# Kernel optimization log

Hardware: AMD Instinct MI355X
Metric: run time of the kernel (lower is better)

Reference implementation:

```python
import jax, jax.numpy as jnp
import numpy as np
import math

D_MODEL = 1024
MEM_SIZE = 4096
N_HEADS = 8
BATCH = 4
SEQ = 1024
TOP_K = min(SEQ, MEM_SIZE // 10)  # 409, matches torch: min(seq_len, memory_size//10)
UPDATE_RATE = 0.01


def _gelu(x):
    return jax.nn.gelu(x, approximate=False)  # torch nn.GELU default (erf)


def setup_inputs() -> dict:
    key = jax.random.key(0)
    ks = jax.random.split(key, 26)
    w = lambda k, shape, s=0.02: (jax.random.normal(k, shape, jnp.float32) * s)
    inp = {
        "x": jax.random.normal(ks[0], (BATCH, SEQ, D_MODEL), jnp.float32),
        "memory_bank": jax.random.normal(ks[1], (MEM_SIZE, D_MODEL), jnp.float32) * 0.1,
        "memory_indices": jax.random.randint(ks[2], (BATCH, TOP_K), 0, MEM_SIZE, jnp.int32),
        # memory_encoder: Linear -> GELU -> Linear
        "enc_w1": w(ks[3], (D_MODEL, D_MODEL)), "enc_b1": jnp.zeros((D_MODEL,), jnp.float32),
        "enc_w2": w(ks[4], (D_MODEL, D_MODEL)), "enc_b2": jnp.zeros((D_MODEL,), jnp.float32),
        # MultiheadAttention in/out projections
        "wq": w(ks[5], (D_MODEL, D_MODEL)), "bq": jnp.zeros((D_MODEL,), jnp.float32),
        "wk": w(ks[6], (D_MODEL, D_MODEL)), "bk": jnp.zeros((D_MODEL,), jnp.float32),
        "wv": w(ks[7], (D_MODEL, D_MODEL)), "bv": jnp.zeros((D_MODEL,), jnp.float32),
        "wo": w(ks[8], (D_MODEL, D_MODEL)), "bo": jnp.zeros((D_MODEL,), jnp.float32),
        # memory_decoder: Linear -> GELU -> Linear
        "dec_w1": w(ks[9], (D_MODEL, D_MODEL)), "dec_b1": jnp.zeros((D_MODEL,), jnp.float32),
        "dec_w2": w(ks[10], (D_MODEL, D_MODEL)), "dec_b2": jnp.zeros((D_MODEL,), jnp.float32),
        # LayerNorm
        "ln_g": jnp.ones((D_MODEL,), jnp.float32), "ln_b": jnp.zeros((D_MODEL,), jnp.float32),
        # importance_scorer: Linear(d,64) -> GELU -> Linear(64,1) -> Sigmoid
        "imp_w1": w(ks[11], (D_MODEL, 64)), "imp_b1": jnp.zeros((64,), jnp.float32),
        "imp_w2": w(ks[12], (64, 1)), "imp_b2": jnp.zeros((1,), jnp.float32),
    }
    return inp


def reference(x, memory_bank, memory_indices,
              enc_w1, enc_b1, enc_w2, enc_b2,
              wq, bq, wk, bk, wv, bv, wo, bo,
              dec_w1, dec_b1, dec_w2, dec_b2,
              ln_g, ln_b, imp_w1, imp_b1, imp_w2, imp_b2):
    B, L, D = x.shape
    M = memory_bank.shape[0]
    H = N_HEADS
    dh = D // H

    # memory_encoder (dropout inactive at eval)
    enc = _gelu(x @ enc_w1 + enc_b1) @ enc_w2 + enc_b2  # [B,L,D]

    # cross-attention: query = encoded input, key/value = memory bank (shared across batch)
    q = (enc @ wq + bq).reshape(B, L, H, dh)
    k = (memory_bank @ wk + bk).reshape(M, H, dh)
    v = (memory_bank @ wv + bv).reshape(M, H, dh)
    scores = jnp.einsum('blhd,mhd->bhlm', q, k) * (1.0 / math.sqrt(dh))
    attn = jax.nn.softmax(scores, axis=-1)                 # [B,H,L,M]
    ctx = jnp.einsum('bhlm,mhd->blhd', attn, v).reshape(B, L, D)
    mem_out = ctx @ wo + bo

    # memory_decoder + residual + LayerNorm
    dec = _gelu(mem_out @ dec_w1 + dec_b1) @ dec_w2 + dec_b2
    comb = x + dec
    mu = jnp.mean(comb, axis=-1, keepdims=True)
    var = jnp.var(comb, axis=-1, keepdims=True)
    out = (comb - mu) / jnp.sqrt(var + 1e-5) * ln_g + ln_b  # [B,L,D]

    # _update_memory: importance top-k select + sequential EMA scatter into memory bank
    imp = jax.nn.sigmoid(_gelu(x @ imp_w1 + imp_b1) @ imp_w2 + imp_b2)[..., 0]  # [B,L]
    _, top_idx = jax.lax.top_k(imp, TOP_K)                  # [B,K]
    top_tok = jnp.take_along_axis(x, top_idx[..., None], axis=1)  # [B,K,D]

    # faithful to the torch double loop (b outer, k inner): sequential EMA with
    # chained updates on index collisions
    flat_idx = memory_indices.reshape(-1)
    flat_tok = top_tok.reshape(-1, D)

    def body(mem, xs):
        i, t = xs
        row = (1.0 - UPDATE_RATE) * mem[i] + UPDATE_RATE * t
        return mem.at[i].set(row), None

    new_mem, _ = jax.lax.scan(body, memory_bank, (flat_idx, flat_tok))
    return out, new_mem
```

## Files before the change

### kernel.cpp

```cpp
#include <hip/hip_runtime.h>

typedef unsigned short u16;
typedef __attribute__((ext_vector_type(4))) int i4;
typedef __attribute__((ext_vector_type(4))) unsigned u4;
typedef __attribute__((ext_vector_type(4))) unsigned short us4;
typedef __attribute__((ext_vector_type(8))) short short8;
typedef __attribute__((ext_vector_type(4))) float f4;

#define D_MODEL 1024
#define ROWS 4096
#define NHEAD 8
#define DH 128
#define TOPK 409
#define NUPD 1636
#define NBATCH 4
#define MAXC 64
#define NPART 2
#define MRANGE 2048
#define ATTNROWS 32768

__device__ __forceinline__ u16 f2bf(float f) {
  unsigned u = __builtin_bit_cast(unsigned, f);
  u += 0x7fffu + ((u >> 16) & 1u);
  return (u16)(u >> 16);
}
__device__ __forceinline__ float bf2f(u16 b) {
  unsigned u = ((unsigned)b) << 16;
  return __builtin_bit_cast(float, u);
}
__device__ __forceinline__ float gelu_f(float v) {
  return 0.5f * v * (1.0f + erff(v * 0.70710678118654752f));
}
__device__ __forceinline__ void gload16(const void* g, void* l) {
  __builtin_amdgcn_global_load_lds((const __attribute__((address_space(1))) void*)g,
                                   (__attribute__((address_space(3))) void*)l, 16, 0, 0);
}

__global__ __launch_bounds__(256) void conv_kernel(const float* __restrict__ in,
                                                   u16* __restrict__ out, int n4) {
  int i = blockIdx.x * 256 + threadIdx.x;
  if (i < n4) {
    f4 v = ((const f4*)in)[i];
    us4 o;
    o.x = f2bf(v.x); o.y = f2bf(v.y); o.z = f2bf(v.z); o.w = f2bf(v.w);
    ((us4*)out)[i] = o;
  }
}

__global__ __launch_bounds__(256) void wtrans8_kernel(const float* s0, const float* s1,
                                                      const float* s2, const float* s3,
                                                      const float* s4, const float* s5,
                                                      const float* s6, const float* s7,
                                                      u16* __restrict__ dst) {
  const float* srcs[8] = {s0, s1, s2, s3, s4, s5, s6, s7};
  const float* w = srcs[blockIdx.z];
  u16* wt = dst + (size_t)blockIdx.z * (1024 * 1024);
  __shared__ float t[32][33];
  int tx = threadIdx.x & 31, ty = threadIdx.x >> 5;
  int k0 = blockIdx.y * 32, n0 = blockIdx.x * 32;
  for (int r = 0; r < 4; ++r)
    t[ty + r * 8][tx] = w[(size_t)(k0 + ty + r * 8) * 1024 + n0 + tx];
  __syncthreads();
  for (int r = 0; r < 4; ++r)
    wt[(size_t)(n0 + ty + r * 8) * 1024 + k0 + tx] = f2bf(t[tx][ty + r * 8]);
}

template <int EPI>
__global__ __launch_bounds__(256) void gemm_bt(const u16* __restrict__ A,
                                               const u16* __restrict__ BT,
                                               const float* __restrict__ bias,
                                               void* __restrict__ C, int M, int N, int K) {
  __shared__ __align__(16) char al[2 * 128 * 64];
  __shared__ __align__(16) char bl[2 * 64 * 64];
  const int tid = threadIdx.x;
  const int lane = tid & 63, wid = tid >> 6;
  const int g = lane >> 4, qi = lane & 15;
  const int m0 = blockIdx.y * 128, n0 = blockIdx.x * 64;
  const int wr = wid >> 1, wc = wid & 1;
  f4 acc[4][2] = {};
  const int nk = K >> 5;

  const int a0r = tid >> 2, a0b = (tid & 3) ^ ((a0r >> 1) & 3);
  const int c1 = tid + 256;
  const int a1r = c1 >> 2, a1b = (c1 & 3) ^ ((a1r >> 1) & 3);
  const int b0r = tid >> 2, b0b = (tid & 3) ^ ((b0r >> 1) & 3);

#define STAGE(buf, kt)                                                                   \
  {                                                                                      \
    const int k0_ = (kt) * 32;                                                           \
    gload16(A + (size_t)(m0 + a0r) * K + k0_ + a0b * 8, al + (buf) * 8192 + tid * 16);   \
    gload16(A + (size_t)(m0 + a1r) * K + k0_ + a1b * 8, al + (buf) * 8192 + c1 * 16);    \
    gload16(BT + (size_t)(n0 + b0r) * K + k0_ + b0b * 8, bl + (buf) * 4096 + tid * 16);  \
  }

  STAGE(0, 0);
  __syncthreads();
  int cur = 0;
  for (int kt = 0; kt < nk; ++kt) {
    if (kt + 1 < nk) STAGE(cur ^ 1, kt + 1);
    short8 af[4], bfr[2];
    for (int i = 0; i < 4; ++i) {
      int r = wr * 64 + i * 16 + qi;
      af[i] = *(const short8*)(al + cur * 8192 + r * 64 + ((g ^ ((r >> 1) & 3))) * 16);
    }
    for (int sn = 0; sn < 2; ++sn) {
      int r = wc * 32 + sn * 16 + qi;
      bfr[sn] = *(const short8*)(bl + cur * 4096 + r * 64 + ((g ^ ((r >> 1) & 3))) * 16);
    }
    for (int i = 0; i < 4; ++i)
      for (int sn = 0; sn < 2; ++sn)
        acc[i][sn] = __builtin_amdgcn_mfma_f32_16x16x32_bf16(af[i], bfr[sn], acc[i][sn], 0, 0, 0);
    __syncthreads();
    cur ^= 1;
  }
#undef STAGE

  for (int i = 0; i < 4; ++i) {
    int row = m0 + wr * 64 + i * 16 + g * 4;
    for (int sn = 0; sn < 2; ++sn) {
      int col = n0 + wc * 32 + sn * 16 + qi;
      float bv = bias[col];
      for (int jj = 0; jj < 4; ++jj) {
        float v = acc[i][sn][jj] + bv;
        if constexpr (EPI == 1) v = gelu_f(v);
        if constexpr (EPI == 2)
          ((float*)C)[(size_t)(row + jj) * N + col] = v;
        else
          ((u16*)C)[(size_t)(row + jj) * N + col] = f2bf(v);
      }
    }
  }
}

__global__ __launch_bounds__(256) void gemm_kv(const u16* __restrict__ A,
                                               const u16* __restrict__ BT,
                                               const float* __restrict__ bk,
                                               const float* __restrict__ bv,
                                               u16* __restrict__ Ck, u16* __restrict__ CvT) {
  __shared__ __align__(16) char pool[2 * 128 * 64 + 2 * 64 * 64];
  char* al = pool;
  char* bl = pool + 2 * 128 * 64;
  const int tid = threadIdx.x;
  const int lane = tid & 63, wid = tid >> 6;
  const int g = lane >> 4, qi = lane & 15;
  const int m0 = blockIdx.y * 128, n0 = blockIdx.x * 64;
  const int wr = wid >> 1, wc = wid & 1;
  const int K = 1024, M = 4096;
  f4 acc[4][2] = {};

  const int a0r = tid >> 2, a0b = (tid & 3) ^ ((a0r >> 1) & 3);
  const int c1 = tid + 256;
  const int a1r = c1 >> 2, a1b = (c1 & 3) ^ ((a1r >> 1) & 3);
  const int b0r = tid >> 2, b0b = (tid & 3) ^ ((b0r >> 1) & 3);

#define STAGE(buf, kt)                                                                   \
  {                                                                                      \
    const int k0_ = (kt) * 32;                                                           \
    gload16(A + (size_t)(m0 + a0r) * K + k0_ + a0b * 8, al + (buf) * 8192 + tid * 16);   \
    gload16(A + (size_t)(m0 + a1r) * K + k0_ + a1b * 8, al + (buf) * 8192 + c1 * 16);    \
    gload16(BT + (size_t)(n0 + b0r) * K + k0_ + b0b * 8, bl + (buf) * 4096 + tid * 16);  \
  }

  STAGE(0, 0);
  __syncthreads();
  int cur = 0;
  for (int kt = 0; kt < 32; ++kt) {
    if (kt + 1 < 32) STAGE(cur ^ 1, kt + 1);
    short8 af[4], bfr[2];
    for (int i = 0; i < 4; ++i) {
      int r = wr * 64 + i * 16 + qi;
      af[i] = *(const short8*)(al + cur * 8192 + r * 64 + ((g ^ ((r >> 1) & 3))) * 16);
    }
    for (int sn = 0; sn < 2; ++sn) {
      int r = wc * 32 + sn * 16 + qi;
      bfr[sn] = *(const short8*)(bl + cur * 4096 + r * 64 + ((g ^ ((r >> 1) & 3))) * 16);
    }
    for (int i = 0; i < 4; ++i)
      for (int sn = 0; sn < 2; ++sn)
        acc[i][sn] = __builtin_amdgcn_mfma_f32_16x16x32_bf16(af[i], bfr[sn], acc[i][sn], 0, 0, 0);
    __syncthreads();
    cur ^= 1;
  }
#undef STAGE

  if (n0 < 1024) {
    for (int i = 0; i < 4; ++i) {
      int row = m0 + wr * 64 + i * 16 + g * 4;
      for (int sn = 0; sn < 2; ++sn) {
        int col = n0 + wc * 32 + sn * 16 + qi;
        float bvv = bk[col];
        for (int jj = 0; jj < 4; ++jj)
          Ck[(size_t)(row + jj) * 1024 + col] = f2bf(acc[i][sn][jj] + bvv);
      }
    }
  } else {
    u16(*t)[132] = (u16(*)[132])pool;
    __syncthreads();
    for (int i = 0; i < 4; ++i)
      for (int sn = 0; sn < 2; ++sn) {
        int nl = wc * 32 + sn * 16 + qi;
        float bvv = bv[n0 - 1024 + nl];
        for (int jj = 0; jj < 4; ++jj)
          t[nl][wr * 64 + i * 16 + g * 4 + jj] = f2bf(acc[i][sn][jj] + bvv);
      }
    __syncthreads();
    int r = tid >> 2, cg = tid & 3;
    for (int v = 0; v < 4; ++v) {
      us4 val = *(const us4*)&t[r][cg * 32 + v * 8];
      *(us4*)&CvT[(size_t)(n0 - 1024 + r) * M + m0 + cg * 32 + v * 8] = val;
    }
  }
}

__global__ __launch_bounds__(512) void attn_kernel(const u16* __restrict__ q,
                                                   const u16* __restrict__ kp,
                                                   const u16* __restrict__ vT,
                                                   u16* __restrict__ ctp,
                                                   float* __restrict__ ml) {
  __shared__ __align__(16) char kl[64 * 256];
  __shared__ __align__(16) char vl[128 * 128];
  const int id = blockIdx.x;
  const int h = id & 7;
  const int rest = id >> 3;
  const int part = rest & 1;
  const int qblk = (rest >> 1) & 7;
  const int b = rest >> 4;
  const int tid = threadIdx.x;
  const int lane = tid & 63, wid = tid >> 6;
  const int g = lane >> 4, qi = lane & 15;
  const int qrow = b * 1024 + qblk * 128 + wid * 16 + qi;
  const float scale = 0.08838834764831845f;

  short8 qf[4];
  for (int kk = 0; kk < 4; ++kk)
    qf[kk] = *(const short8*)(q + (size_t)qrow * 1024 + h * 128 + kk * 32 + g * 8);

  const int kc0 = tid, kc1 = tid + 512;
  const int kr0 = kc0 >> 4, kb0 = kc0 & 15, kr1 = kc1 >> 4, kb1 = kc1 & 15;
  const int vr0 = kc0 >> 3, vb0 = kc0 & 7, vr1 = kc1 >> 3, vb1 = kc1 & 7;
  const int kd0 = kr0 * 256 + (kb0 ^ (kr0 & 7)) * 16;
  const int kd1 = kr1 * 256 + (kb1 ^ (kr1 & 7)) * 16;
  const int vd0 = vr0 * 128 + (vb0 ^ (vr0 & 7)) * 16;
  const int vd1 = vr1 * 128 + (vb1 ^ (vr1 & 7)) * 16;
  const u16* kg0 = kp + (size_t)kr0 * 1024 + h * 128 + kb0 * 8;
  const u16* kg1 = kp + (size_t)kr1 * 1024 + h * 128 + kb1 * 8;
  const u16* vg0 = vT + (size_t)(h * 128 + vr0) * 4096 + vb0 * 8;
  const u16* vg1 = vT + (size_t)(h * 128 + vr1) * 4096 + vb1 * 8;

  i4 kreg0, kreg1, vreg0, vreg1;
  const int mbase = part * MRANGE;
#define LOADREGS(mt_)                                  \
  {                                                    \
    const int m0_ = mbase + (mt_) * 64;                \
    kreg0 = *(const i4*)(kg0 + (size_t)m0_ * 1024);    \
    kreg1 = *(const i4*)(kg1 + (size_t)m0_ * 1024);    \
    vreg0 = *(const i4*)(vg0 + m0_);                   \
    vreg1 = *(const i4*)(vg1 + m0_);                   \
  }

  f4 ct[8] = {};
  float mrun = -1e30f, lsum = 0.0f;

  LOADREGS(0);
  const int nt = MRANGE / 64;
  for (int mt = 0; mt < nt; ++mt) {
    __syncthreads();
    *(i4*)(kl + kd0) = kreg0;
    *(i4*)(kl + kd1) = kreg1;
    *(i4*)(vl + vd0) = vreg0;
    *(i4*)(vl + vd1) = vreg1;
    __syncthreads();
    if (mt + 1 < nt) LOADREGS(mt + 1);

    f4 st[4] = {};
    for (int s = 0; s < 4; ++s) {
      int n = s * 16 + qi;
      const char* krow = kl + n * 256;
      int sw = n & 7;
      for (int kk = 0; kk < 4; ++kk) {
        short8 a = *(const short8*)(krow + ((kk * 4 + g) ^ sw) * 16);
        st[s] = __builtin_amdgcn_mfma_f32_16x16x32_bf16(a, qf[kk], st[s], 0, 0, 0);
      }
    }
    float sv[16];
    float tmax = -1e30f;
    for (int s = 0; s < 4; ++s)
      for (int jj = 0; jj < 4; ++jj) {
        float v = st[s][jj] * scale;
        sv[s * 4 + jj] = v;
        tmax = fmaxf(tmax, v);
      }
    tmax = fmaxf(tmax, __shfl_xor(tmax, 16, 64));
    tmax = fmaxf(tmax, __shfl_xor(tmax, 32, 64));
    float mnew = fmaxf(mrun, tmax);
    float r = __expf(mrun - mnew);
    float psum = 0.0f;
    for (int i = 0; i < 16; ++i) {
      sv[i] = __expf(sv[i] - mnew);
      psum += sv[i];
    }
    psum += __shfl_xor(psum, 16, 64);
    psum += __shfl_xor(psum, 32, 64);
    lsum = lsum * r + psum;
    mrun = mnew;
    for (int i = 0; i < 8; ++i) ct[i] = ct[i] * r;

    unsigned pk0[4], pk1[4];
    for (int s = 0; s < 4; ++s) {
      pk0[s] = (unsigned)f2bf(sv[s * 4 + 0]) | ((unsigned)f2bf(sv[s * 4 + 1]) << 16);
      pk1[s] = (unsigned)f2bf(sv[s * 4 + 2]) | ((unsigned)f2bf(sv[s * 4 + 3]) << 16);
    }
    const int src1 = qi + ((g & 1) << 5);
    const int src2 = src1 + 16;
    const bool hi = (g & 2) != 0;
    for (int p = 0; p < 2; ++p) {
      unsigned a0 = __shfl(pk0[2 * p], src1, 64), b0 = __shfl(pk0[2 * p + 1], src1, 64);
      unsigned a1 = __shfl(pk1[2 * p], src1, 64), b1 = __shfl(pk1[2 * p + 1], src1, 64);
      unsigned a2 = __shfl(pk0[2 * p], src2, 64), b2 = __shfl(pk0[2 * p + 1], src2, 64);
      unsigned a3 = __shfl(pk1[2 * p], src2, 64), b3 = __shfl(pk1[2 * p + 1], src2, 64);
      u4 bw;
      bw.x = hi ? b0 : a0; bw.y = hi ? b1 : a1; bw.z = hi ? b2 : a2; bw.w = hi ? b3 : a3;
      short8 pf = __builtin_bit_cast(short8, bw);
      for (int d = 0; d < 8; ++d) {
        int dr = d * 16 + qi;
        short8 a = *(const short8*)(vl + dr * 128 + (((p * 4 + g) ^ (dr & 7))) * 16);
        ct[d] = __builtin_amdgcn_mfma_f32_16x16x32_bf16(a, pf, ct[d], 0, 0, 0);
      }
    }
  }
#undef LOADREGS

  const int orow = ((b * 8 + h) << 10) + qblk * 128 + wid * 16 + qi;
  if (g == 0) {
    ml[(size_t)(part * ATTNROWS + orow) * 2 + 0] = mrun;
    ml[(size_t)(part * ATTNROWS + orow) * 2 + 1] = lsum;
  }
  for (int d = 0; d < 8; ++d) {
    us4 o;
    o.x = f2bf(ct[d][0]); o.y = f2bf(ct[d][1]);
    o.z = f2bf(ct[d][2]); o.w = f2bf(ct[d][3]);
    *(us4*)(ctp + ((size_t)(part * ATTNROWS + orow)) * 128 + d * 16 + g * 4) = o;
  }
}

__global__ __launch_bounds__(256) void combine_kernel(const u16* __restrict__ ctp,
                                                      const float* __restrict__ ml,
                                                      u16* __restrict__ ctx) {
  int tid = threadIdx.x;
  int row = blockIdx.x * 16 + (tid >> 4);
  int dp = (tid & 15) * 8;
  float m0 = ml[(size_t)row * 2], l0 = ml[(size_t)row * 2 + 1];
  float m1 = ml[(size_t)(ATTNROWS + row) * 2], l1 = ml[(size_t)(ATTNROWS + row) * 2 + 1];
  float m = fmaxf(m0, m1);
  float s0 = __expf(m0 - m), s1 = __expf(m1 - m);
  float inv = 1.0f / (l0 * s0 + l1 * s1);
  short8 c0 = *(const short8*)(ctp + (size_t)row * 128 + dp);
  short8 c1 = *(const short8*)(ctp + (size_t)(ATTNROWS + row) * 128 + dp);
  us4 o[2];
  for (int i = 0; i < 8; ++i) {
    float f = (bf2f((u16)c0[i]) * s0 + bf2f((u16)c1[i]) * s1) * inv;
    ((u16*)o)[i] = f2bf(f);
  }
  int bb = row >> 13, hh = (row >> 10) & 7, qr = row & 1023;
  *(short8*)(ctx + (size_t)((bb << 10) + qr) * 1024 + hh * 128 + dp) =
      __builtin_bit_cast(short8, o);
}

__global__ __launch_bounds__(256) void ln_kernel(const float* __restrict__ x,
                                                 const float* __restrict__ dec,
                                                 const float* __restrict__ gw,
                                                 const float* __restrict__ bw,
                                                 float* __restrict__ out,
                                                 int* __restrict__ cnt) {
  __shared__ float rs[256], rs2[256];
  int row = blockIdx.x, tid = threadIdx.x;
  if (tid == 0) cnt[row] = 0;
  float c[4];
  float s = 0.0f, s2 = 0.0f;
  for (int i = 0; i < 4; ++i) {
    int col = tid + i * 256;
    float v = x[(size_t)row * 1024 + col] + dec[(size_t)row * 1024 + col];
    c[i] = v; s += v; s2 += v * v;
  }
  rs[tid] = s; rs2[tid] = s2;
  __syncthreads();
  for (int st = 128; st > 0; st >>= 1) {
    if (tid < st) { rs[tid] += rs[tid + st]; rs2[tid] += rs2[tid + st]; }
    __syncthreads();
  }
  float mu = rs[0] * (1.0f / 1024.0f);
  float var = rs2[0] * (1.0f / 1024.0f) - mu * mu;
  float inv = rsqrtf(var + 1e-5f);
  for (int i = 0; i < 4; ++i) {
    int col = tid + i * 256;
    out[(size_t)row * 1024 + col] = (c[i] - mu) * inv * gw[col] + bw[col];
  }
}

__global__ __launch_bounds__(256) void imp_kernel(const float* __restrict__ x,
                                                  const float* __restrict__ w1,
                                                  const float* __restrict__ b1,
                                                  const float* __restrict__ w2,
                                                  const float* __restrict__ b2,
                                                  float* __restrict__ imp) {
  __shared__ float xs[8][1024];
  int tid = threadIdx.x;
  int lane = tid & 63, wid = tid >> 6;
  size_t base = (size_t)blockIdx.x * 8192;
  for (int i = 0; i < 32; ++i) ((float*)xs)[tid + i * 256] = x[base + tid + i * 256];
  __syncthreads();
  int r0 = wid * 2, r1 = wid * 2 + 1;
  float a0 = 0.0f, a1 = 0.0f;
  for (int k = 0; k < 1024; ++k) {
    float wv = w1[k * 64 + lane];
    a0 += xs[r0][k] * wv;
    a1 += xs[r1][k] * wv;
  }
  float h0 = gelu_f(a0 + b1[lane]) * w2[lane];
  float h1 = gelu_f(a1 + b1[lane]) * w2[lane];
  for (int d = 1; d < 64; d <<= 1) {
    h0 += __shfl_xor(h0, d, 64);
    h1 += __shfl_xor(h1, d, 64);
  }
  if (lane == 0) {
    imp[blockIdx.x * 8 + r0] = 1.0f / (1.0f + expf(-(h0 + b2[0])));
    imp[blockIdx.x * 8 + r1] = 1.0f / (1.0f + expf(-(h1 + b2[0])));
  }
}

__global__ __launch_bounds__(512) void topk_kernel(const float* __restrict__ imp,
                                                   int* __restrict__ tidx) {
  __shared__ float v[1024];
  __shared__ int ix[1024];
  int b = blockIdx.x, tid = threadIdx.x;
  for (int i = tid; i < 1024; i += 512) { v[i] = imp[b * 1024 + i]; ix[i] = i; }
  __syncthreads();
  for (int k = 2; k <= 1024; k <<= 1) {
    for (int j = k >> 1; j > 0; j >>= 1) {
      for (int t = tid; t < 1024; t += 512) {
        int p = t ^ j;
        if (p > t) {
          float va = v[t], vb = v[p];
          int ia = ix[t], ib = ix[p];
          bool ord = (va > vb) || (va == vb && ia < ib);
          bool up = ((t & k) == 0);
          if (up ? !ord : ord) { v[t] = vb; v[p] = va; ix[t] = ib; ix[p] = ia; }
        }
      }
      __syncthreads();
    }
  }
  for (int t = tid; t < TOPK; t += 512) tidx[b * TOPK + t] = ix[t];
}

__global__ __launch_bounds__(128) void rank_kernel(const int* __restrict__ midx,
                                                   int* __restrict__ cnt,
                                                   int* __restrict__ slot) {
  __shared__ int mi[NUPD];
  int tid = threadIdx.x;
  for (int i = tid; i < NUPD; i += 128) mi[i] = midx[i];
  __syncthreads();
  int j = blockIdx.x * 128 + tid;
  if (j < NUPD) {
    int r = mi[j], rank = 0;
    for (int jp = 0; jp < j; ++jp) rank += (mi[jp] == r) ? 1 : 0;
    if (rank < MAXC) slot[r * MAXC + rank] = j;
    atomicAdd(&cnt[r], 1);
  }
}

__global__ __launch_bounds__(256) void apply_kernel(const float* __restrict__ x,
                                                    const float* __restrict__ mem,
                                                    const int* __restrict__ tidx,
                                                    const int* __restrict__ cnt,
                                                    const int* __restrict__ slot,
                                                    float* __restrict__ outm) {
  int row = blockIdx.x, tid = threadIdx.x;
  f4 acc = ((const f4*)(mem + (size_t)row * 1024))[tid];
  int c = cnt[row];
  c = c < MAXC ? c : MAXC;
  for (int t = 0; t < c; ++t) {
    int j = slot[row * MAXC + t];
    int b = j / TOPK;
    int tr = tidx[j];
    f4 xv = ((const f4*)(x + ((size_t)b * 1024 + tr) * 1024))[tid];
    acc = acc * 0.99f + xv * 0.01f;
  }
  ((f4*)(outm + (size_t)row * 1024))[tid] = acc;
}

extern "C" void kernel_launch(void* const* d_in, const int* in_sizes, int n_in,
                              void* d_out, int out_size, void* d_ws, size_t ws_size,
                              hipStream_t stream) {
  const float* x = (const float*)d_in[0];
  const float* memory_bank = (const float*)d_in[1];
  const int* memory_indices = (const int*)d_in[2];
  const float* enc_w1 = (const float*)d_in[3];
  const float* enc_b1 = (const float*)d_in[4];
  const float* enc_w2 = (const float*)d_in[5];
  const float* enc_b2 = (const float*)d_in[6];
  const float* wq = (const float*)d_in[7];
  const float* bq = (const float*)d_in[8];
  const float* wk = (const float*)d_in[9];
  const float* bk = (const float*)d_in[10];
  const float* wv = (const float*)d_in[11];
  const float* bv = (const float*)d_in[12];
  const float* wo = (const float*)d_in[13];
  const float* bo = (const float*)d_in[14];
  const float* dec_w1 = (const float*)d_in[15];
  const float* dec_b1 = (const float*)d_in[16];
  const float* dec_w2 = (const float*)d_in[17];
  const float* dec_b2 = (const float*)d_in[18];
  const float* ln_g = (const float*)d_in[19];
  const float* ln_b = (const float*)d_in[20];
  const float* imp_w1 = (const float*)d_in[21];
  const float* imp_b1 = (const float*)d_in[22];
  const float* imp_w2 = (const float*)d_in[23];
  const float* imp_b2 = (const float*)d_in[24];

  char* ws = (char*)d_ws;
  u16* buf0 = (u16*)(ws);
  u16* buf1 = (u16*)(ws + (8ull << 20));
  u16* buf2 = (u16*)(ws + (16ull << 20));
  u16* buf3 = (u16*)(ws + (24ull << 20));
  u16* buf4 = (u16*)(ws + (32ull << 20));
  float* decb = (float*)(ws + (40ull << 20));
  u16* wtb = (u16*)(ws + (56ull << 20));
  float* impb = (float*)(ws + (72ull << 20));
  int* tidx = (int*)(ws + (72ull << 20) + (1 << 16));
  u16* ctp = (u16*)decb;
  float* ml = (float*)buf0;
  int* cnt = (int*)buf3;
  int* slot = (int*)(ws + (24ull << 20) + (1 << 16));

  const int NM = 1024 * 1024;
  u16* wt_e1 = wtb + 0 * NM;
  u16* wt_e2 = wtb + 1 * NM;
  u16* wt_q = wtb + 2 * NM;
  u16* wt_k = wtb + 3 * NM;
  u16* wt_o = wtb + 5 * NM;
  u16* wt_d1 = wtb + 6 * NM;
  u16* wt_d2 = wtb + 7 * NM;

  conv_kernel<<<4096, 256, 0, stream>>>(x, buf0, ROWS * D_MODEL / 4);
  conv_kernel<<<4096, 256, 0, stream>>>(memory_bank, buf2, ROWS * D_MODEL / 4);

  wtrans8_kernel<<<dim3(32, 32, 8), 256, 0, stream>>>(enc_w1, enc_w2, wq, wk, wv, wo,
                                                      dec_w1, dec_w2, wtb);

  dim3 gg(16, 32);
  gemm_bt<1><<<gg, 256, 0, stream>>>(buf0, wt_e1, enc_b1, buf1, ROWS, 1024, 1024);
  gemm_bt<0><<<gg, 256, 0, stream>>>(buf1, wt_e2, enc_b2, buf0, ROWS, 1024, 1024);
  gemm_bt<0><<<gg, 256, 0, stream>>>(buf0, wt_q, bq, buf1, ROWS, 1024, 1024);
  gemm_kv<<<dim3(32, 32), 256, 0, stream>>>(buf2, wt_k, bk, bv, buf3, buf4);
  attn_kernel<<<512, 512, 0, stream>>>(buf1, buf3, buf4, ctp, ml);
  combine_kernel<<<2048, 256, 0, stream>>>(ctp, ml, buf2);
  gemm_bt<0><<<gg, 256, 0, stream>>>(buf2, wt_o, bo, buf0, ROWS, 1024, 1024);
  gemm_bt<1><<<gg, 256, 0, stream>>>(buf0, wt_d1, dec_b1, buf1, ROWS, 1024, 1024);
  gemm_bt<2><<<gg, 256, 0, stream>>>(buf1, wt_d2, dec_b2, decb, ROWS, 1024, 1024);
  ln_kernel<<<4096, 256, 0, stream>>>(x, decb, ln_g, ln_b, (float*)d_out, cnt);
  imp_kernel<<<512, 256, 0, stream>>>(x, imp_w1, imp_b1, imp_w2, imp_b2, impb);
  topk_kernel<<<NBATCH, 512, 0, stream>>>(impb, tidx);
  rank_kernel<<<13, 128, 0, stream>>>(memory_indices, cnt, slot);
  apply_kernel<<<4096, 256, 0, stream>>>(x, memory_bank, tidx, cnt, slot,
                                         (float*)d_out + (size_t)ROWS * D_MODEL);
}
```

Before: 425.7 us.

## Split attention over four memory partitions and remap GEMM blocks per XCD

Attention now splits the 4096 memory rows into four partitions instead of two. This doubles the number of blocks so more work is in flight across the CUs, and a new four-way combine kernel merges the partial results using their max and sum statistics. The GEMM and KV-projection kernels switch to a 1D grid whose block index is remapped so that blocks landing on the same XCD share A-row tiles, aiming for better L2 reuse; M, N and K become compile-time constants. The cost is extra partial-output traffic and a heavier combine step, plus workspace buffers reused as aliases that must not overlap live data.

After: 442.2 us. +3.9%, slower.

```diff
diff --git a/kernel.cpp b/kernel.cpp
--- a/kernel.cpp
+++ b/kernel.cpp
@@ -15,8 +15,6 @@
 #define NUPD 1636
 #define NBATCH 4
 #define MAXC 64
-#define NPART 2
-#define MRANGE 2048
 #define ATTNROWS 32768
 
 __device__ __forceinline__ u16 f2bf(float f) {
@@ -69,16 +67,19 @@
 __global__ __launch_bounds__(256) void gemm_bt(const u16* __restrict__ A,
                                                const u16* __restrict__ BT,
                                                const float* __restrict__ bias,
-                                               void* __restrict__ C, int M, int N, int K) {
+                                               void* __restrict__ C) {
   __shared__ __align__(16) char al[2 * 128 * 64];
   __shared__ __align__(16) char bl[2 * 64 * 64];
+  const int K = 1024, N = 1024;
+  const int id = blockIdx.x;
+  const int xcd = id & 7, j = id >> 3;
+  const int m0 = ((j & 3) * 8 + xcd) * 128;
+  const int n0 = (j >> 2) * 64;
   const int tid = threadIdx.x;
   const int lane = tid & 63, wid = tid >> 6;
   const int g = lane >> 4, qi = lane & 15;
-  const int m0 = blockIdx.y * 128, n0 = blockIdx.x * 64;
   const int wr = wid >> 1, wc = wid & 1;
   f4 acc[4][2] = {};
-  const int nk = K >> 5;
 
   const int a0r = tid >> 2, a0b = (tid & 3) ^ ((a0r >> 1) & 3);
   const int c1 = tid + 256;
@@ -96,8 +97,8 @@
   STAGE(0, 0);
   __syncthreads();
   int cur = 0;
-  for (int kt = 0; kt < nk; ++kt) {
-    if (kt + 1 < nk) STAGE(cur ^ 1, kt + 1);
+  for (int kt = 0; kt < 32; ++kt) {
+    if (kt + 1 < 32) STAGE(cur ^ 1, kt + 1);
     short8 af[4], bfr[2];
     for (int i = 0; i < 4; ++i) {
       int r = wr * 64 + i * 16 + qi;
@@ -140,10 +141,13 @@
   __shared__ __align__(16) char pool[2 * 128 * 64 + 2 * 64 * 64];
   char* al = pool;
   char* bl = pool + 2 * 128 * 64;
+  const int id = blockIdx.x;
+  const int xcd = id & 7, j = id >> 3;
+  const int m0 = ((j & 3) * 8 + xcd) * 128;
+  const int n0 = (j >> 2) * 64;
   const int tid = threadIdx.x;
   const int lane = tid & 63, wid = tid >> 6;
   const int g = lane >> 4, qi = lane & 15;
-  const int m0 = blockIdx.y * 128, n0 = blockIdx.x * 64;
   const int wr = wid >> 1, wc = wid & 1;
   const int K = 1024, M = 4096;
   f4 acc[4][2] = {};
@@ -212,24 +216,29 @@
   }
 }
 
+template <int LP>
 __global__ __launch_bounds__(512) void attn_kernel(const u16* __restrict__ q,
                                                    const u16* __restrict__ kp,
                                                    const u16* __restrict__ vT,
-                                                   u16* __restrict__ ctp,
+                                                   u16* __restrict__ cp0, u16* __restrict__ cp1,
+                                                   u16* __restrict__ cp2, u16* __restrict__ cp3,
                                                    float* __restrict__ ml) {
+  constexpr int MR = 4096 >> LP;
+  constexpr int NT = MR / 64;
   __shared__ __align__(16) char kl[64 * 256];
   __shared__ __align__(16) char vl[128 * 128];
   const int id = blockIdx.x;
   const int h = id & 7;
   const int rest = id >> 3;
-  const int part = rest & 1;
-  const int qblk = (rest >> 1) & 7;
-  const int b = rest >> 4;
+  const int part = rest & ((1 << LP) - 1);
+  const int qblk = (rest >> LP) & 7;
+  const int b = rest >> (3 + LP);
   const int tid = threadIdx.x;
   const int lane = tid & 63, wid = tid >> 6;
   const int g = lane >> 4, qi = lane & 15;
   const int qrow = b * 1024 + qblk * 128 + wid * 16 + qi;
   const float scale = 0.08838834764831845f;
+  u16* ctp = (part == 0) ? cp0 : (part == 1) ? cp1 : (part == 2) ? cp2 : cp3;
 
   short8 qf[4];
   for (int kk = 0; kk < 4; ++kk)
@@ -242,13 +251,13 @@
   const int kd1 = kr1 * 256 + (kb1 ^ (kr1 & 7)) * 16;
   const int vd0 = vr0 * 128 + (vb0 ^ (vr0 & 7)) * 16;
   const int vd1 = vr1 * 128 + (vb1 ^ (vr1 & 7)) * 16;
+  const int mbase = part * MR;
   const u16* kg0 = kp + (size_t)kr0 * 1024 + h * 128 + kb0 * 8;
   const u16* kg1 = kp + (size_t)kr1 * 1024 + h * 128 + kb1 * 8;
   const u16* vg0 = vT + (size_t)(h * 128 + vr0) * 4096 + vb0 * 8;
   const u16* vg1 = vT + (size_t)(h * 128 + vr1) * 4096 + vb1 * 8;
 
   i4 kreg0, kreg1, vreg0, vreg1;
-  const int mbase = part * MRANGE;
 #define LOADREGS(mt_)                                  \
   {                                                    \
     const int m0_ = mbase + (mt_) * 64;                \
@@ -262,15 +271,14 @@
   float mrun = -1e30f, lsum = 0.0f;
 
   LOADREGS(0);
-  const int nt = MRANGE / 64;
-  for (int mt = 0; mt < nt; ++mt) {
+  for (int mt = 0; mt < NT; ++mt) {
     __syncthreads();
     *(i4*)(kl + kd0) = kreg0;
     *(i4*)(kl + kd1) = kreg1;
     *(i4*)(vl + vd0) = vreg0;
     *(i4*)(vl + vd1) = vreg1;
     __syncthreads();
-    if (mt + 1 < nt) LOADREGS(mt + 1);
+    if (mt + 1 < NT) LOADREGS(mt + 1);
 
     f4 st[4] = {};
     for (int s = 0; s < 4; ++s) {
@@ -339,26 +347,34 @@
     us4 o;
     o.x = f2bf(ct[d][0]); o.y = f2bf(ct[d][1]);
     o.z = f2bf(ct[d][2]); o.w = f2bf(ct[d][3]);
-    *(us4*)(ctp + ((size_t)(part * ATTNROWS + orow)) * 128 + d * 16 + g * 4) = o;
-  }
-}
-
-__global__ __launch_bounds__(256) void combine_kernel(const u16* __restrict__ ctp,
-                                                      const float* __restrict__ ml,
-                                                      u16* __restrict__ ctx) {
+    *(us4*)(ctp + (size_t)orow * 128 + d * 16 + g * 4) = o;
+  }
+}
+
+__global__ __launch_bounds__(256) void combine4_kernel(const u16* __restrict__ cp0,
+                                                       const u16* __restrict__ cp1,
+                                                       const u16* __restrict__ cp2,
+                                                       const u16* __restrict__ cp3,
+                                                       const float* __restrict__ ml,
+                                                       u16* __restrict__ ctx) {
   int tid = threadIdx.x;
   int row = blockIdx.x * 16 + (tid >> 4);
   int dp = (tid & 15) * 8;
   float m0 = ml[(size_t)row * 2], l0 = ml[(size_t)row * 2 + 1];
-  float m1 = ml[(size_t)(ATTNROWS + row) * 2], l1 = ml[(size_t)(ATTNROWS + row) * 2 + 1];
-  float m = fmaxf(m0, m1);
-  float s0 = __expf(m0 - m), s1 = __expf(m1 - m);
-  float inv = 1.0f / (l0 * s0 + l1 * s1);
-  short8 c0 = *(const short8*)(ctp + (size_t)row * 128 + dp);
-  short8 c1 = *(const short8*)(ctp + (size_t)(ATTNROWS + row) * 128 + dp);
+  float m1 = ml[((size_t)ATTNROWS + row) * 2], l1 = ml[((size_t)ATTNROWS + row) * 2 + 1];
+  float m2 = ml[((size_t)2 * ATTNROWS + row) * 2], l2 = ml[((size_t)2 * ATTNROWS + row) * 2 + 1];
+  float m3 = ml[((size_t)3 * ATTNROWS + row) * 2], l3 = ml[((size_t)3 * ATTNROWS + row) * 2 + 1];
+  float m = fmaxf(fmaxf(m0, m1), fmaxf(m2, m3));
+  float s0 = __expf(m0 - m), s1 = __expf(m1 - m), s2 = __expf(m2 - m), s3 = __expf(m3 - m);
+  float inv = 1.0f / (l0 * s0 + l1 * s1 + l2 * s2 + l3 * s3);
+  short8 c0 = *(const short8*)(cp0 + (size_t)row * 128 + dp);
+  short8 c1 = *(const short8*)(cp1 + (size_t)row * 128 + dp);
+  short8 c2 = *(const short8*)(cp2 + (size_t)row * 128 + dp);
+  short8 c3 = *(const short8*)(cp3 + (size_t)row * 128 + dp);
   us4 o[2];
   for (int i = 0; i < 8; ++i) {
-    float f = (bf2f((u16)c0[i]) * s0 + bf2f((u16)c1[i]) * s1) * inv;
+    float f = (bf2f((u16)c0[i]) * s0 + bf2f((u16)c1[i]) * s1 + bf2f((u16)c2[i]) * s2 +
+               bf2f((u16)c3[i]) * s3) * inv;
     ((u16*)o)[i] = f2bf(f);
   }
   int bb = row >> 13, hh = (row >> 10) & 7, qr = row & 1023;
@@ -528,10 +544,13 @@
   u16* wtb = (u16*)(ws + (56ull << 20));
   float* impb = (float*)(ws + (72ull << 20));
   int* tidx = (int*)(ws + (72ull << 20) + (1 << 16));
-  u16* ctp = (u16*)decb;
-  float* ml = (float*)buf0;
   int* cnt = (int*)buf3;
   int* slot = (int*)(ws + (24ull << 20) + (1 << 16));
+  u16* cp0 = buf0;
+  u16* cp1 = buf2;
+  u16* cp2 = (u16*)(ws + (40ull << 20));
+  u16* cp3 = (u16*)(ws + (48ull << 20));
+  float* ml = (float*)(ws + (56ull << 20));
 
   const int NM = 1024 * 1024;
   u16* wt_e1 = wtb + 0 * NM;
@@ -544,21 +563,22 @@
 
   conv_kernel<<<4096, 256, 0, stream>>>(x, buf0, ROWS * D_MODEL / 4);
   conv_kernel<<<4096, 256, 0, stream>>>(memory_bank, buf2, ROWS * D_MODEL / 4);
-
   wtrans8_kernel<<<dim3(32, 32, 8), 256, 0, stream>>>(enc_w1, enc_w2, wq, wk, wv, wo,
                                                       dec_w1, dec_w2, wtb);
 
-  dim3 gg(16, 32);
-  gemm_bt<1><<<gg, 256, 0, stream>>>(buf0, wt_e1, enc_b1, buf1, ROWS, 1024, 1024);
-  gemm_bt<0><<<gg, 256, 0, stream>>>(buf1, wt_e2, enc_b2, buf0, ROWS, 1024, 1024);
-  gemm_bt<0><<<gg, 256, 0, stream>>>(buf0, wt_q, bq, buf1, ROWS, 1024, 1024);
-  gemm_kv<<<dim3(32, 32), 256, 0, stream>>>(buf2, wt_k, bk, bv, buf3, buf4);
-  attn_kernel<<<512, 512, 0, stream>>>(buf1, buf3, buf4, ctp, ml);
-  combine_kernel<<<2048, 256, 0, stream>>>(ctp, ml, buf2);
-  gemm_bt<0><<<gg, 256, 0, stream>>>(buf2, wt_o, bo, buf0, ROWS, 1024, 1024);
-  gemm_bt<1><<<gg, 256, 0, stream>>>(buf0, wt_d1, dec_b1, buf1, ROWS, 1024, 1024);
-  gemm_bt<2><<<gg, 256, 0, stream>>>(buf1, wt_d2, dec_b2, decb, ROWS, 1024, 1024);
+  gemm_bt<1><<<512, 256, 0, stream>>>(buf0, wt_e1, enc_b1, buf1);
+  gemm_bt<0><<<512, 256, 0, stream>>>(buf1, wt_e2, enc_b2, buf0);
+  gemm_bt<0><<<512, 256, 0, stream>>>(buf0, wt_q, bq, buf1);
+  gemm_kv<<<1024, 256, 0, stream>>>(buf2, wt_k, bk, bv, buf3, buf4);
+
+  attn_kernel<2><<<1024, 512, 0, stream>>>(buf1, buf3, buf4, cp0, cp1, cp2, cp3, ml);
+  combine4_kernel<<<2048, 256, 0, stream>>>(cp0, cp1, cp2, cp3, ml, buf1);
+
+  gemm_bt<0><<<512, 256, 0, stream>>>(buf1, wt_o, bo, buf0);
+  gemm_bt<1><<<512, 256, 0, stream>>>(buf0, wt_d1, dec_b1, buf2);
+  gemm_bt<2><<<512, 256, 0, stream>>>(buf2, wt_d2, dec_b2, decb);
   ln_kernel<<<4096, 256, 0, stream>>>(x, decb, ln_g, ln_b, (float*)d_out, cnt);
+
   imp_kernel<<<512, 256, 0, stream>>>(x, imp_w1, imp_b1, imp_w2, imp_b2, impb);
   topk_kernel<<<NBATCH, 512, 0, stream>>>(impb, tidx);
   rank_kernel<<<13, 128, 0, stream>>>(memory_indices, cnt, slot);
```
